# Performance work log

Hardware: AMD Instinct MI355X
Metric: run time of the kernel (lower is better)

The kernel has to match this reference:

```python
import jax, jax.numpy as jnp
import numpy as np

SYMMETRIC = True
NORMED = True

# (distance, angle) -> pixel offsets (row, col) exactly as in the original:
# row = round(sin(angle))*d, col = round(cos(angle))*d for angles 0, pi/4, pi/2, 3pi/4
OFFSETS = [(0, 1), (1, 1), (1, 0), (1, -1),
           (0, 2), (2, 2), (2, 0), (2, -2),
           (0, 3), (3, 3), (3, 0), (3, -3)]


def setup_inputs() -> dict:
    key = jax.random.key(0)
    inputs = jax.random.normal(key, (128, 512, 512, 1), dtype=jnp.float32)
    return {"inputs": inputs}


def _glcm_one(img, row, col):
    # img: binarized [B,H,W,C]
    B, H, W, C = img.shape
    if col > 0:
        a = img[:, :H - row, :W - col, :]
        b = img[:, row:, col:, :]
    else:
        # -0 slice == full width, matching the original Keras code
        a = img[:, :H - row, -col:, :]
        b = img[:, row:, :W + col, :]
    axes = (1, 2, 3)
    a_or_b = jnp.maximum(a, b)
    a_and_b = a * b
    M00 = jnp.sum(1.0 - a_or_b, axis=axes)           # [B]
    M01 = jnp.sum(b * (1.0 - a), axis=axes)
    M10 = jnp.sum(a * (1.0 - b), axis=axes)
    M11 = jnp.sum(a_and_b, axis=axes)
    if SYMMETRIC:
        temp = jnp.stack([M00 * 2.0, M01 + M10, M01 + M10, M11 * 2.0], axis=1)  # [B,4]
    else:
        temp = jnp.stack([M00, M01, M10, M11], axis=1)
    if NORMED:
        temp = temp / jnp.sum(temp, axis=1, keepdims=True)
    return temp


def reference(inputs) -> jnp.ndarray:
    # Binarize once (original redundantly re-binarizes per glcm pass; same math).
    img = jnp.sign(inputs)
    outs = [_glcm_one(img, r, c) for (r, c) in OFFSETS]
    return jnp.concatenate(outs, axis=1)  # [B, 48]
```

## Files before the change

kernel.cpp:

```cpp
#include <hip/hip_runtime.h>
#include <stdint.h>

#define BATCH 128
#define HH 512
#define WW 512
#define NTILES (BATCH * HH * 2)
#define PACK_BLOCKS 2048
#define PACK_WAVES (PACK_BLOCKS * 4)
#define TILES_PER_WAVE (NTILES / PACK_WAVES)
#define PITCH 10

__global__ __launch_bounds__(256) void pack_signs(const float* __restrict__ img,
                                                  uint64_t* __restrict__ mask) {
    int wid = (int)blockIdx.x * 4 + ((int)threadIdx.x >> 6);
    int lane = (int)threadIdx.x & 63;
#pragma unroll 4
    for (int it = 0; it < TILES_PER_WAVE; ++it) {
        int tile = wid + it * PACK_WAVES;
        const float4 v = *(const float4*)(img + (size_t)tile * 256 + lane * 4);
        uint64_t m0 = __ballot(v.x < 0.f);
        uint64_t m1 = __ballot(v.y < 0.f);
        uint64_t m2 = __ballot(v.z < 0.f);
        uint64_t m3 = __ballot(v.w < 0.f);
        if (lane == 0) {
            ulonglong4 st;
            st.x = m0; st.y = m1; st.z = m2; st.w = m3;
            *(ulonglong4*)(mask + (size_t)tile * 4) = st;
        }
    }
}

__device__ __forceinline__ uint32_t popc8(const uint64_t* R) {
    uint32_t s = 0;
#pragma unroll
    for (int w = 0; w < 8; ++w) s += (uint32_t)__popcll(R[w]);
    return s;
}

__device__ __forceinline__ void shiftdn(const uint64_t* R, int sh, uint64_t* S) {
#pragma unroll
    for (int t8 = 0; t8 < 2; ++t8)
#pragma unroll
        for (int k = 0; k < 4; ++k) {
            int kc = k + sh;
            if (kc < 4) {
                S[t8 * 4 + k] = R[t8 * 4 + kc];
            } else {
                uint64_t x = R[t8 * 4 + kc - 4] >> 1;
                if (t8 == 0) x |= R[4 + kc - 4] << 63;
                S[t8 * 4 + k] = x;
            }
        }
}

__device__ __forceinline__ void procC(const uint64_t* A, const uint64_t* B, int c,
                                      uint32_t* acc) {
    int sh = c > 0 ? c : -c;
    uint64_t S[8];
    uint32_t oa = 0, ob = 0, on = 0;
    if (c > 0) {
        shiftdn(B, sh, S);
#pragma unroll
        for (int w = 0; w < 8; ++w) {
            uint64_t a = A[w];
            uint64_t am = ((w >> 2) == 1 && (w & 3) >= 4 - sh) ? (a & ~(1ull << 63)) : a;
            oa += (uint32_t)__popcll(am);
            ob += (uint32_t)__popcll(S[w]);
            on += (uint32_t)__popcll(a & S[w]);
        }
    } else {
        shiftdn(A, sh, S);
#pragma unroll
        for (int w = 0; w < 8; ++w) {
            uint64_t bb = B[w];
            uint64_t bm = ((w >> 2) == 1 && (w & 3) >= 4 - sh) ? (bb & ~(1ull << 63)) : bb;
            oa += (uint32_t)__popcll(S[w]);
            ob += (uint32_t)__popcll(bm);
            on += (uint32_t)__popcll(S[w] & bb);
        }
    }
    acc[0] += oa; acc[1] += ob; acc[2] += on;
}

__device__ __forceinline__ void proc0(const uint64_t* A, const uint64_t* B,
                                      uint32_t rpA, uint32_t rpB, uint32_t* acc) {
    uint32_t on = 0;
#pragma unroll
    for (int w = 0; w < 8; ++w) on += (uint32_t)__popcll(A[w] & B[w]);
    acc[0] += rpA; acc[1] += rpB; acc[2] += on;
}

__device__ __forceinline__ void loadrow(const uint64_t* lds, int y, uint64_t* R) {
#pragma unroll
    for (int i = 0; i < 4; ++i)
        *(ulonglong2*)&R[2 * i] = *(const ulonglong2*)&lds[y * PITCH + 2 * i];
}

__global__ __launch_bounds__(256) void glcm_bits(const uint64_t* __restrict__ mask,
                                                 float* __restrict__ out) {
    __shared__ uint64_t lds[HH * PITCH];
    __shared__ uint32_t partial[4][36];
    int b = (int)blockIdx.x;
    int t = (int)threadIdx.x;
    const uint64_t* mb = mask + (size_t)b * (HH * 8);

#pragma unroll
    for (int i = 0; i < 8; ++i) {
        int g = i * 256 + t;
        ulonglong2 v = ((const ulonglong2*)mb)[g];
        int row = g >> 2;
        int w2 = (g & 3) << 1;
        *(ulonglong2*)&lds[row * PITCH + w2] = v;
    }
    __syncthreads();

    uint32_t acc[12][3];
#pragma unroll
    for (int j = 0; j < 12; ++j) { acc[j][0] = 0; acc[j][1] = 0; acc[j][2] = 0; }

#pragma unroll
    for (int yy = 0; yy < 2; ++yy) {
        int y = t + yy * 256;
        uint64_t A[8];
        loadrow(lds, y, A);
        uint32_t rpA = popc8(A);
        procC(A, A, 1, acc[0]);
        procC(A, A, 2, acc[4]);
        procC(A, A, 3, acc[8]);
        uint64_t Brow[8];
        if (y + 1 < HH) {
            loadrow(lds, y + 1, Brow);
            uint32_t rpB = popc8(Brow);
            procC(A, Brow, 1, acc[1]);
            proc0(A, Brow, rpA, rpB, acc[2]);
            procC(A, Brow, -1, acc[3]);
        }
        if (y + 2 < HH) {
            loadrow(lds, y + 2, Brow);
            uint32_t rpB = popc8(Brow);
            procC(A, Brow, 2, acc[5]);
            proc0(A, Brow, rpA, rpB, acc[6]);
            procC(A, Brow, -2, acc[7]);
        }
        if (y + 3 < HH) {
            loadrow(lds, y + 3, Brow);
            uint32_t rpB = popc8(Brow);
            procC(A, Brow, 3, acc[9]);
            proc0(A, Brow, rpA, rpB, acc[10]);
            procC(A, Brow, -3, acc[11]);
        }
    }

    int lane = t & 63, wv = t >> 6;
#pragma unroll
    for (int j = 0; j < 12; ++j)
#pragma unroll
        for (int q = 0; q < 3; ++q) {
            int v = (int)acc[j][q];
            for (int m = 32; m >= 1; m >>= 1) v += __shfl_xor(v, m, 64);
            acc[j][q] = (uint32_t)v;
        }
    if (lane == 0) {
#pragma unroll
        for (int j = 0; j < 12; ++j) {
            partial[wv][j * 3 + 0] = acc[j][0];
            partial[wv][j * 3 + 1] = acc[j][1];
            partial[wv][j * 3 + 2] = acc[j][2];
        }
    }
    __syncthreads();

    if (t < 12) {
        const int rtab[12] = {0, 1, 1, 1, 0, 2, 2, 2, 0, 3, 3, 3};
        const int ctab[12] = {1, 1, 0, -1, 2, 2, 0, -2, 3, 3, 0, -3};
        uint32_t oa = 0, ob = 0, on = 0;
#pragma unroll
        for (int w = 0; w < 4; ++w) {
            oa += partial[w][t * 3 + 0];
            ob += partial[w][t * 3 + 1];
            on += partial[w][t * 3 + 2];
        }
        int r = rtab[t];
        int sh = ctab[t] < 0 ? -ctab[t] : ctab[t];
        float Nwin = (float)((HH - r) * (WW - sh));
        float foa = (float)oa, fob = (float)ob, fon = (float)on;
        float e0 = 4.f * fon;
        float e1 = 2.f * (foa + fob) - 8.f * fon;
        float e3 = 2.f * Nwin - 4.f * (foa + fob) + 8.f * fon;
        float inv = 1.0f / (2.f * Nwin - 4.f * fon);
        float4 o;
        o.x = e0 * inv; o.y = e1 * inv; o.z = e1 * inv; o.w = e3 * inv;
        *(float4*)(out + (size_t)b * 48 + t * 4) = o;
    }
}

extern "C" void kernel_launch(void* const* d_in, const int* in_sizes, int n_in,
                              void* d_out, int out_size, void* d_ws, size_t ws_size,
                              hipStream_t stream) {
    const float* img = (const float*)d_in[0];
    float* out = (float*)d_out;
    uint64_t* mask = (uint64_t*)d_ws;
    (void)in_sizes; (void)n_in; (void)out_size; (void)ws_size;

    pack_signs<<<dim3(PACK_BLOCKS), dim3(256), 0, stream>>>(img, mask);
    glcm_bits<<<dim3(BATCH), dim3(256), 0, stream>>>(mask, out);
}
```

Before: 34.97 us.

## Fuse sign packing into banded GLCM kernel with halo rows and partial reduction

```diff
diff --git a/kernel.cpp b/kernel.cpp
--- a/kernel.cpp
+++ b/kernel.cpp
@@ -4,31 +4,10 @@
 #define BATCH 128
 #define HH 512
 #define WW 512
-#define NTILES (BATCH * HH * 2)
-#define PACK_BLOCKS 2048
-#define PACK_WAVES (PACK_BLOCKS * 4)
-#define TILES_PER_WAVE (NTILES / PACK_WAVES)
+#define BAND 64
+#define NB (HH / BAND)
+#define HALO 3
 #define PITCH 10
-
-__global__ __launch_bounds__(256) void pack_signs(const float* __restrict__ img,
-                                                  uint64_t* __restrict__ mask) {
-    int wid = (int)blockIdx.x * 4 + ((int)threadIdx.x >> 6);
-    int lane = (int)threadIdx.x & 63;
-#pragma unroll 4
-    for (int it = 0; it < TILES_PER_WAVE; ++it) {
-        int tile = wid + it * PACK_WAVES;
-        const float4 v = *(const float4*)(img + (size_t)tile * 256 + lane * 4);
-        uint64_t m0 = __ballot(v.x < 0.f);
-        uint64_t m1 = __ballot(v.y < 0.f);
-        uint64_t m2 = __ballot(v.z < 0.f);
-        uint64_t m3 = __ballot(v.w < 0.f);
-        if (lane == 0) {
-            ulonglong4 st;
-            st.x = m0; st.y = m1; st.z = m2; st.w = m3;
-            *(ulonglong4*)(mask + (size_t)tile * 4) = st;
-        }
-    }
-}
 
 __device__ __forceinline__ uint32_t popc8(const uint64_t* R) {
     uint32_t s = 0;
@@ -37,7 +16,7 @@
     return s;
 }
 
-__device__ __forceinline__ void shiftdn(const uint64_t* R, int sh, uint64_t* S) {
+__device__ __forceinline__ void shiftdn(const uint64_t* R, const int sh, uint64_t* S) {
 #pragma unroll
     for (int t8 = 0; t8 < 2; ++t8)
 #pragma unroll
@@ -53,9 +32,9 @@
         }
 }
 
-__device__ __forceinline__ void procC(const uint64_t* A, const uint64_t* B, int c,
+__device__ __forceinline__ void procC(const uint64_t* A, const uint64_t* B, const int c,
                                       uint32_t* acc) {
-    int sh = c > 0 ? c : -c;
+    const int sh = c > 0 ? c : -c;
     uint64_t S[8];
     uint32_t oa = 0, ob = 0, on = 0;
     if (c > 0) {
@@ -96,94 +75,128 @@
         *(ulonglong2*)&R[2 * i] = *(const ulonglong2*)&lds[y * PITCH + 2 * i];
 }
 
-__global__ __launch_bounds__(256) void glcm_bits(const uint64_t* __restrict__ mask,
+__device__ __forceinline__ void pack_half(const float* base, int yg, int half, int lane,
+                                          uint64_t* lds, int row) {
+    const float4 v = *(const float4*)(base + (size_t)yg * WW + half * 256 + lane * 4);
+    uint64_t m0 = __ballot(v.x < 0.f);
+    uint64_t m1 = __ballot(v.y < 0.f);
+    uint64_t m2 = __ballot(v.z < 0.f);
+    uint64_t m3 = __ballot(v.w < 0.f);
+    if (lane == 0) {
+        uint64_t* p = &lds[row * PITCH + half * 4];
+        ulonglong2 s0, s1;
+        s0.x = m0; s0.y = m1; s1.x = m2; s1.y = m3;
+        *(ulonglong2*)&p[0] = s0;
+        *(ulonglong2*)&p[2] = s1;
+    }
+}
+
+__global__ __launch_bounds__(256) void glcm_fused(const float* __restrict__ img,
+                                                  uint32_t* __restrict__ part) {
+    __shared__ uint64_t lds[(BAND + HALO) * PITCH];
+    __shared__ uint32_t xw[4][9];
+    int blk = (int)blockIdx.x;
+    int band = blk & (NB - 1);
+    int b = blk >> 3;
+    int y0 = band * BAND;
+    int t = (int)threadIdx.x, lane = t & 63, wv = t >> 6;
+    const float* base = img + (size_t)b * HH * WW;
+
+    int nrows = min(BAND + HALO, HH - y0);
+    int ntasks = nrows * 2;
+
+    int id = wv;
+    while (id + 4 < ntasks) {
+        int r0 = id >> 1, h0 = id & 1;
+        int r1 = (id + 4) >> 1, h1 = (id + 4) & 1;
+        pack_half(base, y0 + r0, h0, lane, lds, r0);
+        pack_half(base, y0 + r1, h1, lane, lds, r1);
+        id += 8;
+    }
+    if (id < ntasks) pack_half(base, y0 + (id >> 1), id & 1, lane, lds, id >> 1);
+    __syncthreads();
+
+    uint32_t acc[3][3];
+#pragma unroll
+    for (int o = 0; o < 3; ++o) { acc[o][0] = 0; acc[o][1] = 0; acc[o][2] = 0; }
+
+    int r = lane;
+    uint64_t A[8];
+    loadrow(lds, r, A);
+
+    if (wv == 0) {
+        procC(A, A, 1, acc[0]);
+        procC(A, A, 2, acc[1]);
+        procC(A, A, 3, acc[2]);
+    } else if (wv == 1) {
+        if (y0 + r + 1 < HH) {
+            uint64_t B[8];
+            loadrow(lds, r + 1, B);
+            uint32_t rpA = popc8(A), rpB = popc8(B);
+            procC(A, B, 1, acc[0]);
+            proc0(A, B, rpA, rpB, acc[1]);
+            procC(A, B, -1, acc[2]);
+        }
+    } else if (wv == 2) {
+        if (y0 + r + 2 < HH) {
+            uint64_t B[8];
+            loadrow(lds, r + 2, B);
+            uint32_t rpA = popc8(A), rpB = popc8(B);
+            procC(A, B, 2, acc[0]);
+            proc0(A, B, rpA, rpB, acc[1]);
+            procC(A, B, -2, acc[2]);
+        }
+    } else {
+        if (y0 + r + 3 < HH) {
+            uint64_t B[8];
+            loadrow(lds, r + 3, B);
+            uint32_t rpA = popc8(A), rpB = popc8(B);
+            procC(A, B, 3, acc[0]);
+            proc0(A, B, rpA, rpB, acc[1]);
+            procC(A, B, -3, acc[2]);
+        }
+    }
+
+#pragma unroll
+    for (int o = 0; o < 3; ++o)
+#pragma unroll
+        for (int q = 0; q < 3; ++q) {
+            int v = (int)acc[o][q];
+            for (int m = 32; m >= 1; m >>= 1) v += __shfl_xor(v, m, 64);
+            acc[o][q] = (uint32_t)v;
+        }
+    if (lane == 0) {
+        const int jt[4][3] = {{0, 4, 8}, {1, 2, 3}, {5, 6, 7}, {9, 10, 11}};
+        uint32_t* pb = part + (size_t)blk * 36;
+#pragma unroll
+        for (int o = 0; o < 3; ++o)
+#pragma unroll
+            for (int q = 0; q < 3; ++q) pb[jt[wv][o] * 3 + q] = acc[o][q];
+    }
+}
+
+__global__ __launch_bounds__(64) void glcm_final(const uint32_t* __restrict__ part,
                                                  float* __restrict__ out) {
-    __shared__ uint64_t lds[HH * PITCH];
-    __shared__ uint32_t partial[4][36];
+    __shared__ uint32_t sums[36];
     int b = (int)blockIdx.x;
     int t = (int)threadIdx.x;
-    const uint64_t* mb = mask + (size_t)b * (HH * 8);
-
-#pragma unroll
-    for (int i = 0; i < 8; ++i) {
-        int g = i * 256 + t;
-        ulonglong2 v = ((const ulonglong2*)mb)[g];
-        int row = g >> 2;
-        int w2 = (g & 3) << 1;
-        *(ulonglong2*)&lds[row * PITCH + w2] = v;
+    if (t < 36) {
+        uint32_t s = 0;
+        const uint32_t* p = part + (size_t)b * NB * 36 + t;
+#pragma unroll
+        for (int k = 0; k < NB; ++k) s += p[k * 36];
+        sums[t] = s;
     }
     __syncthreads();
-
-    uint32_t acc[12][3];
-#pragma unroll
-    for (int j = 0; j < 12; ++j) { acc[j][0] = 0; acc[j][1] = 0; acc[j][2] = 0; }
-
-#pragma unroll
-    for (int yy = 0; yy < 2; ++yy) {
-        int y = t + yy * 256;
-        uint64_t A[8];
-        loadrow(lds, y, A);
-        uint32_t rpA = popc8(A);
-        procC(A, A, 1, acc[0]);
-        procC(A, A, 2, acc[4]);
-        procC(A, A, 3, acc[8]);
-        uint64_t Brow[8];
-        if (y + 1 < HH) {
-            loadrow(lds, y + 1, Brow);
-            uint32_t rpB = popc8(Brow);
-            procC(A, Brow, 1, acc[1]);
-            proc0(A, Brow, rpA, rpB, acc[2]);
-            procC(A, Brow, -1, acc[3]);
-        }
-        if (y + 2 < HH) {
-            loadrow(lds, y + 2, Brow);
-            uint32_t rpB = popc8(Brow);
-            procC(A, Brow, 2, acc[5]);
-            proc0(A, Brow, rpA, rpB, acc[6]);
-            procC(A, Brow, -2, acc[7]);
-        }
-        if (y + 3 < HH) {
-            loadrow(lds, y + 3, Brow);
-            uint32_t rpB = popc8(Brow);
-            procC(A, Brow, 3, acc[9]);
-            proc0(A, Brow, rpA, rpB, acc[10]);
-            procC(A, Brow, -3, acc[11]);
-        }
-    }
-
-    int lane = t & 63, wv = t >> 6;
-#pragma unroll
-    for (int j = 0; j < 12; ++j)
-#pragma unroll
-        for (int q = 0; q < 3; ++q) {
-            int v = (int)acc[j][q];
-            for (int m = 32; m >= 1; m >>= 1) v += __shfl_xor(v, m, 64);
-            acc[j][q] = (uint32_t)v;
-        }
-    if (lane == 0) {
-#pragma unroll
-        for (int j = 0; j < 12; ++j) {
-            partial[wv][j * 3 + 0] = acc[j][0];
-            partial[wv][j * 3 + 1] = acc[j][1];
-            partial[wv][j * 3 + 2] = acc[j][2];
-        }
-    }
-    __syncthreads();
-
     if (t < 12) {
         const int rtab[12] = {0, 1, 1, 1, 0, 2, 2, 2, 0, 3, 3, 3};
         const int ctab[12] = {1, 1, 0, -1, 2, 2, 0, -2, 3, 3, 0, -3};
-        uint32_t oa = 0, ob = 0, on = 0;
-#pragma unroll
-        for (int w = 0; w < 4; ++w) {
-            oa += partial[w][t * 3 + 0];
-            ob += partial[w][t * 3 + 1];
-            on += partial[w][t * 3 + 2];
-        }
         int r = rtab[t];
         int sh = ctab[t] < 0 ? -ctab[t] : ctab[t];
+        float foa = (float)sums[t * 3 + 0];
+        float fob = (float)sums[t * 3 + 1];
+        float fon = (float)sums[t * 3 + 2];
         float Nwin = (float)((HH - r) * (WW - sh));
-        float foa = (float)oa, fob = (float)ob, fon = (float)on;
         float e0 = 4.f * fon;
         float e1 = 2.f * (foa + fob) - 8.f * fon;
         float e3 = 2.f * Nwin - 4.f * (foa + fob) + 8.f * fon;
@@ -199,9 +212,9 @@
                               hipStream_t stream) {
     const float* img = (const float*)d_in[0];
     float* out = (float*)d_out;
-    uint64_t* mask = (uint64_t*)d_ws;
+    uint32_t* part = (uint32_t*)d_ws;
     (void)in_sizes; (void)n_in; (void)out_size; (void)ws_size;
 
-    pack_signs<<<dim3(PACK_BLOCKS), dim3(256), 0, stream>>>(img, mask);
-    glcm_bits<<<dim3(BATCH), dim3(256), 0, stream>>>(mask, out);
-}
+    glcm_fused<<<dim3(BATCH * NB), dim3(256), 0, stream>>>(img, part);
+    glcm_final<<<dim3(BATCH), dim3(64), 0, stream>>>(part, out);
+}
```

Result: faster. 30.21 us (-13.6%).
